# Optimization experiments

Hardware: AMD Instinct MI355X
Metric: run time of the kernel (lower is better)

## Reference

```python
import jax, jax.numpy as jnp
import numpy as np

B, T, D, H = 64, 512, 1024, 1024


def setup_inputs() -> dict:
    key = jax.random.key(0)
    k1, k2, k3 = jax.random.split(key, 3)
    scale = 0.02  # keep tanh out of saturation
    return {
        "x": jax.random.normal(k1, (B, T, D), dtype=jnp.float32),
        "Wi": jax.random.normal(k2, (H, D), dtype=jnp.float32) * scale,
        "bi": jnp.zeros((H,), dtype=jnp.float32),
        "Wh": jax.random.normal(k3, (H, H), dtype=jnp.float32) * scale,
        "bh": jnp.zeros((H,), dtype=jnp.float32),
    }


def reference(x, Wi, bi, Wh, bh):
    # x: [B, T, D]; torch Linear weights are [out, in].
    # Precompute the input projection as one big GEMM (faithful: Wi(x_t)+bi).
    xi = jnp.einsum("btd,hd->bth", x, Wi) + bi  # [B, T, H]

    def step(h, xt):
        # h: [B, H], xt: [B, H]
        h_new = jnp.tanh(xt + h @ Wh.T + bh)
        return h_new, h_new

    h0 = jnp.zeros((x.shape[0], Wh.shape[0]), dtype=x.dtype)
    _, hs = jax.lax.scan(step, h0, jnp.swapaxes(xi, 0, 1))  # [T, B, H]
    return jnp.swapaxes(hs, 0, 1)  # [B, T, H]
```

## Files before the change

kernel.cpp:

```cpp
#include <hip/hip_runtime.h>
#include <hip/hip_bf16.h>

#define B_ 64
#define T_ 512
#define D_ 1024
#define H_ 1024

typedef __bf16 bf16x8 __attribute__((ext_vector_type(8)));
typedef float f32x4 __attribute__((ext_vector_type(4)));

static __device__ __forceinline__ unsigned short f2bf(float f) {
  union { float f; unsigned u; } v; v.f = f;
  unsigned u = v.u;
  unsigned r = (u + 0x7fffu + ((u >> 16) & 1u)) >> 16;
  return (unsigned short)r;
}

__global__ __launch_bounds__(256) void xi_gemm(const float* __restrict__ x,
                                               const float* __restrict__ Wi,
                                               const float* __restrict__ bi,
                                               float* __restrict__ out) {
  __shared__ __align__(16) unsigned short As[128][40];
  __shared__ __align__(16) unsigned short Ws[128][40];
  const int tid = threadIdx.x;
  const int wave = tid >> 6;
  const int lane = tid & 63;
  const int wm = wave >> 1, wn = wave & 1;
  const int lr = lane & 15, lk = lane >> 4;
  const long row0 = (long)blockIdx.x * 128;
  const int col0 = (int)blockIdx.y * 128;

  f32x4 acc[4][4];
#pragma unroll
  for (int m = 0; m < 4; ++m)
#pragma unroll
    for (int n = 0; n < 4; ++n)
      acc[m][n] = (f32x4){0.f, 0.f, 0.f, 0.f};

  for (int kt = 0; kt < 32; ++kt) {
    __syncthreads();
#pragma unroll
    for (int it = 0; it < 4; ++it) {
      int i = tid + it * 256;
      int row = i >> 3, c = i & 7;
      float4 va = *reinterpret_cast<const float4*>(
          &x[(row0 + row) * 1024 + kt * 32 + c * 4]);
      ushort4 ba = {f2bf(va.x), f2bf(va.y), f2bf(va.z), f2bf(va.w)};
      *reinterpret_cast<ushort4*>(&As[row][c * 4]) = ba;
      float4 vw = *reinterpret_cast<const float4*>(
          &Wi[(long)(col0 + row) * 1024 + kt * 32 + c * 4]);
      ushort4 bw = {f2bf(vw.x), f2bf(vw.y), f2bf(vw.z), f2bf(vw.w)};
      *reinterpret_cast<ushort4*>(&Ws[row][c * 4]) = bw;
    }
    __syncthreads();
    bf16x8 af[4], wf[4];
#pragma unroll
    for (int m = 0; m < 4; ++m)
      af[m] = *reinterpret_cast<const bf16x8*>(&As[wm * 64 + m * 16 + lr][lk * 8]);
#pragma unroll
    for (int n = 0; n < 4; ++n)
      wf[n] = *reinterpret_cast<const bf16x8*>(&Ws[wn * 64 + n * 16 + lr][lk * 8]);
#pragma unroll
    for (int m = 0; m < 4; ++m)
#pragma unroll
      for (int n = 0; n < 4; ++n)
        acc[m][n] = __builtin_amdgcn_mfma_f32_16x16x32_bf16(af[m], wf[n], acc[m][n], 0, 0, 0);
  }
#pragma unroll
  for (int m = 0; m < 4; ++m) {
#pragma unroll
    for (int n = 0; n < 4; ++n) {
#pragma unroll
      for (int r = 0; r < 4; ++r) {
        long row = row0 + wm * 64 + m * 16 + lk * 4 + r;
        int col = col0 + wn * 64 + n * 16 + lr;
        out[row * 1024 + col] = acc[m][n][r] + bi[col];
      }
    }
  }
}

__global__ __launch_bounds__(64) void rnn_xcd(const float* __restrict__ Wh,
                                              const float* __restrict__ bh,
                                              float* __restrict__ out,
                                              unsigned* __restrict__ ctrs,
                                              unsigned* __restrict__ flagsF,
                                              unsigned* __restrict__ flagsB,
                                              unsigned short* __restrict__ hsF,
                                              unsigned short* __restrict__ hsB) {
  extern __shared__ __align__(16) unsigned short Whs[];
  const int lane = threadIdx.x;
  const int lr = lane & 15, lk = lane >> 4;

  unsigned xcc = 0, slot = 0, okv = 0;
  if (lane == 0) {
    xcc = __builtin_amdgcn_s_getreg((31u << 11) | 20u) & 15u;
    slot = __hip_atomic_fetch_add(&ctrs[xcc], 1u, __ATOMIC_RELAXED,
                                  __HIP_MEMORY_SCOPE_AGENT);
    __hip_atomic_fetch_add(&ctrs[16], 1u, __ATOMIC_RELEASE,
                           __HIP_MEMORY_SCOPE_AGENT);
    unsigned spin = 0;
    while (__hip_atomic_load(&ctrs[16], __ATOMIC_ACQUIRE,
                             __HIP_MEMORY_SCOPE_AGENT) < 256u) {
      __builtin_amdgcn_s_sleep(1);
      if (++spin > 2000000u) break;
    }
    unsigned ok = 1;
    for (int i = 0; i < 8; ++i)
      if (__hip_atomic_load(&ctrs[i], __ATOMIC_RELAXED,
                            __HIP_MEMORY_SCOPE_AGENT) != 32u) ok = 0;
    for (int i = 8; i < 16; ++i)
      if (__hip_atomic_load(&ctrs[i], __ATOMIC_RELAXED,
                            __HIP_MEMORY_SCOPE_AGENT) != 0u) ok = 0;
    okv = ok;
  }
  xcc  = (unsigned)__shfl((int)xcc, 0, 64);
  slot = (unsigned)__shfl((int)slot, 0, 64);
  okv  = (unsigned)__shfl((int)okv, 0, 64);

  if (okv) {
    const int j0 = (int)slot * 32;
#pragma unroll 8
    for (int it = 0; it < 128; ++it) {
      int i = lane + it * 64;
      int row = i >> 8, c = i & 255;
      float4 v = *reinterpret_cast<const float4*>(&Wh[(long)(j0 + row) * 1024 + c * 4]);
      ushort4 b4 = {f2bf(v.x), f2bf(v.y), f2bf(v.z), f2bf(v.w)};
      *reinterpret_cast<ushort4*>(&Whs[row * 1032 + c * 4]) = b4;
    }
    __syncthreads();

    const int jc0 = j0 + lr;
    const int jc1 = j0 + 16 + lr;
    const float bhv0 = bh[jc0], bhv1 = bh[jc1];
    const unsigned short* wb0 = &Whs[lr * 1032 + lk * 8];
    const unsigned short* wb1 = &Whs[(16 + lr) * 1032 + lk * 8];
    unsigned* hw = reinterpret_cast<unsigned*>(hsF);
    const unsigned fslot = (xcc * 32u + slot) << 4;

    for (int t = 0; t < T_; ++t) {
      float xr0[4], xr1[4];
      if (t > 0) {
        asm volatile("s_waitcnt vmcnt(0)" ::: "memory");
        if (lane == 0)
          __hip_atomic_store(&flagsF[fslot], (unsigned)t,
                             __ATOMIC_RELAXED, __HIP_MEMORY_SCOPE_AGENT);
        if (lk < 2) {
#pragma unroll
          for (int r = 0; r < 4; ++r) {
            size_t oi = ((size_t)(xcc * 8 + lk * 4 + r) * T_ + t) * H_;
            xr0[r] = out[oi + jc0];
            xr1[r] = out[oi + jc1];
          }
        }
        unsigned spin = 0;
        for (;;) {
          unsigned v = (unsigned)t;
          if (lane < 32)
            v = __hip_atomic_load(&flagsF[(xcc * 32u + (unsigned)lane) << 4],
                                  __ATOMIC_RELAXED, __HIP_MEMORY_SCOPE_AGENT);
          if (__all((int)(v >= (unsigned)t))) break;
          if (spin >= 2) __builtin_amdgcn_s_sleep(1);
          if (++spin > 50000u) break;
        }
        __builtin_amdgcn_fence(__ATOMIC_ACQUIRE, "agent");
      } else {
        if (lk < 2) {
#pragma unroll
          for (int r = 0; r < 4; ++r) {
            size_t oi = ((size_t)(xcc * 8 + lk * 4 + r) * T_ + t) * H_;
            xr0[r] = out[oi + jc0];
            xr1[r] = out[oi + jc1];
          }
        }
      }

      f32x4 a00 = {0,0,0,0}, a01 = {0,0,0,0}, a10 = {0,0,0,0}, a11 = {0,0,0,0};
      if (t > 0) {
        const unsigned short* hp = hsF + (size_t)xcc * 32768 +
                                   (size_t)((t - 1) & 1) * 16384 +
                                   (size_t)lr * 1024 + lk * 8;
#pragma unroll 4
        for (int ks = 0; ks < 16; ++ks) {
          bf16x8 ah0 = *reinterpret_cast<const bf16x8*>(hp + ks * 32);
          bf16x8 ah1 = *reinterpret_cast<const bf16x8*>(hp + (ks + 16) * 32);
          bf16x8 w00 = *reinterpret_cast<const bf16x8*>(wb0 + ks * 32);
          bf16x8 w01 = *reinterpret_cast<const bf16x8*>(wb0 + (ks + 16) * 32);
          bf16x8 w10 = *reinterpret_cast<const bf16x8*>(wb1 + ks * 32);
          bf16x8 w11 = *reinterpret_cast<const bf16x8*>(wb1 + (ks + 16) * 32);
          a00 = __builtin_amdgcn_mfma_f32_16x16x32_bf16(ah0, w00, a00, 0, 0, 0);
          a01 = __builtin_amdgcn_mfma_f32_16x16x32_bf16(ah1, w01, a01, 0, 0, 0);
          a10 = __builtin_amdgcn_mfma_f32_16x16x32_bf16(ah0, w10, a10, 0, 0, 0);
          a11 = __builtin_amdgcn_mfma_f32_16x16x32_bf16(ah1, w11, a11, 0, 0, 0);
        }
      }
      f32x4 acc0 = a00 + a01, acc1 = a10 + a11;

      const unsigned pw = (unsigned)(t & 1) * 8192u;
      if (lk < 2) {
#pragma unroll
        for (int r = 0; r < 4; ++r) {
          int row = lk * 4 + r;
          size_t oi = ((size_t)(xcc * 8 + row) * T_ + t) * H_;
          float h0 = tanhf(xr0[r] + acc0[r] + bhv0);
          float h1 = tanhf(xr1[r] + acc1[r] + bhv1);
          out[oi + jc0] = h0;
          out[oi + jc1] = h1;
          unsigned u0 = f2bf(h0), u1 = f2bf(h1);
          unsigned o0 = (unsigned)__shfl_xor((int)u0, 1, 64);
          unsigned o1 = (unsigned)__shfl_xor((int)u1, 1, 64);
          if ((lr & 1) == 0) {
            unsigned base = xcc * 16384u + pw + (unsigned)row * 512u;
            hw[base + ((unsigned)jc0 >> 1)] = u0 | (o0 << 16);
            hw[base + ((unsigned)jc1 >> 1)] = u1 | (o1 << 16);
          }
        }
      }
    }
  } else {
    const int bid = (int)blockIdx.x;
    const int jg = bid & 63, bg = bid >> 6;
    const int j0 = jg * 16, brow = bg * 16;
#pragma unroll 8
    for (int it = 0; it < 64; ++it) {
      int i = lane + it * 64;
      int row = i >> 8, c = i & 255;
      float4 v = *reinterpret_cast<const float4*>(&Wh[(long)(j0 + row) * 1024 + c * 4]);
      ushort4 b4 = {f2bf(v.x), f2bf(v.y), f2bf(v.z), f2bf(v.w)};
      *reinterpret_cast<ushort4*>(&Whs[row * 1032 + c * 4]) = b4;
    }
    __syncthreads();
    const int jcol = j0 + lr;
    const float bhv = bh[jcol];
    const unsigned short* wbl = &Whs[lr * 1032 + lk * 8];
    unsigned* hw = reinterpret_cast<unsigned*>(hsB);
    const int jp = jcol >> 1;

    for (int t = 0; t < T_; ++t) {
      if (t > 0) {
        asm volatile("s_waitcnt vmcnt(0)" ::: "memory");
        if (lane == 0)
          __hip_atomic_store(&flagsB[(unsigned)bid << 4], (unsigned)t,
                             __ATOMIC_RELAXED, __HIP_MEMORY_SCOPE_AGENT);
        unsigned spin = 0;
        for (;;) {
          unsigned va = __hip_atomic_load(&flagsB[(unsigned)lane << 4],
                                 __ATOMIC_RELAXED, __HIP_MEMORY_SCOPE_AGENT);
          unsigned vb = __hip_atomic_load(&flagsB[((unsigned)lane + 64u) << 4],
                                 __ATOMIC_RELAXED, __HIP_MEMORY_SCOPE_AGENT);
          unsigned vc = __hip_atomic_load(&flagsB[((unsigned)lane + 128u) << 4],
                                 __ATOMIC_RELAXED, __HIP_MEMORY_SCOPE_AGENT);
          unsigned vd = __hip_atomic_load(&flagsB[((unsigned)lane + 192u) << 4],
                                 __ATOMIC_RELAXED, __HIP_MEMORY_SCOPE_AGENT);
          int ok = (va >= (unsigned)t) && (vb >= (unsigned)t) &&
                   (vc >= (unsigned)t) && (vd >= (unsigned)t);
          if (__all(ok)) break;
          __builtin_amdgcn_s_sleep(2);
          if (++spin > 50000u) break;
        }
        __builtin_amdgcn_fence(__ATOMIC_ACQUIRE, "agent");
      }

      f32x4 a0 = {0,0,0,0}, a1 = {0,0,0,0};
      if (t > 0) {
        const unsigned short* hbl = hsB + (size_t)((t - 1) & 1) * 65536 +
                                    (size_t)(brow + lr) * 1024 + lk * 8;
#pragma unroll 4
        for (int ks = 0; ks < 16; ++ks) {
          bf16x8 ah0 = *reinterpret_cast<const bf16x8*>(hbl + ks * 32);
          bf16x8 ah1 = *reinterpret_cast<const bf16x8*>(hbl + (ks + 16) * 32);
          bf16x8 wf0 = *reinterpret_cast<const bf16x8*>(wbl + ks * 32);
          bf16x8 wf1 = *reinterpret_cast<const bf16x8*>(wbl + (ks + 16) * 32);
          a0 = __builtin_amdgcn_mfma_f32_16x16x32_bf16(ah0, wf0, a0, 0, 0, 0);
          a1 = __builtin_amdgcn_mfma_f32_16x16x32_bf16(ah1, wf1, a1, 0, 0, 0);
        }
      }
      f32x4 acc = a0 + a1;

      const unsigned pw = (unsigned)(t & 1) * 32768u;
#pragma unroll
      for (int r = 0; r < 4; ++r) {
        int b = brow + lk * 4 + r;
        size_t oi = ((size_t)b * T_ + t) * H_ + jcol;
        float z = out[oi] + acc[r] + bhv;
        float h = tanhf(z);
        out[oi] = h;
        unsigned hi_u = f2bf(h);
        unsigned o_hi = (unsigned)__shfl_xor((int)hi_u, 1, 64);
        if ((lr & 1) == 0) {
          __hip_atomic_store(&hw[pw + (unsigned)b * 512u + (unsigned)jp],
                             hi_u | (o_hi << 16),
                             __ATOMIC_RELAXED, __HIP_MEMORY_SCOPE_AGENT);
        }
      }
    }
  }
}

__global__ __launch_bounds__(256) void rnn_step(const float* __restrict__ Wh,
                                                const float* __restrict__ bh,
                                                float* __restrict__ out,
                                                int t) {
  const int bg = blockIdx.x & 3;
  const int jg = blockIdx.x >> 2;
  const int b = bg * 16 + (threadIdx.x >> 4);
  const int j = jg * 16 + (threadIdx.x & 15);
  float a0 = 0.f, a1 = 0.f, a2 = 0.f, a3 = 0.f;
  if (t > 0) {
    const float4* __restrict__ wr = reinterpret_cast<const float4*>(&Wh[(long)j * H_]);
    const float4* __restrict__ hr = reinterpret_cast<const float4*>(
        &out[((long)b * T_ + (t - 1)) * H_]);
#pragma unroll 8
    for (int kc = 0; kc < 256; ++kc) {
      float4 w = wr[kc];
      float4 h = hr[kc];
      a0 = fmaf(w.x, h.x, a0);
      a1 = fmaf(w.y, h.y, a1);
      a2 = fmaf(w.z, h.z, a2);
      a3 = fmaf(w.w, h.w, a3);
    }
  }
  const long oi = ((long)b * T_ + t) * H_ + j;
  float z = out[oi] + ((a0 + a1) + (a2 + a3)) + bh[j];
  out[oi] = tanhf(z);
}

extern "C" void kernel_launch(void* const* d_in, const int* in_sizes, int n_in,
                              void* d_out, int out_size, void* d_ws, size_t ws_size,
                              hipStream_t stream) {
  const float* x  = (const float*)d_in[0];
  const float* Wi = (const float*)d_in[1];
  const float* bi = (const float*)d_in[2];
  const float* Wh = (const float*)d_in[3];
  const float* bh = (const float*)d_in[4];
  float* out = (float*)d_out;

  const size_t CTRS_OFF  = 0;
  const size_t FLAGF_OFF = 4096;
  const size_t FLAGB_OFF = 20480;
  const size_t HSF_OFF   = 36864;
  const size_t HSB_OFF   = 561152;
  const size_t NEED      = HSB_OFF + 262144;

  hipLaunchKernelGGL(xi_gemm, dim3(256, 8), dim3(256), 0, stream, x, Wi, bi, out);

  bool launched = false;
  if (ws_size >= NEED) {
    unsigned* ctrs = (unsigned*)((char*)d_ws + CTRS_OFF);
    unsigned* flagsF = (unsigned*)((char*)d_ws + FLAGF_OFF);
    unsigned* flagsB = (unsigned*)((char*)d_ws + FLAGB_OFF);
    unsigned short* hsF = (unsigned short*)((char*)d_ws + HSF_OFF);
    unsigned short* hsB = (unsigned short*)((char*)d_ws + HSB_OFF);
    hipMemsetAsync(d_ws, 0, HSF_OFF + 524288, stream);

    const float* Wh_ = Wh; const float* bh_ = bh; float* out_ = out;
    void* args[] = {(void*)&Wh_, (void*)&bh_, (void*)&out_,
                    (void*)&ctrs, (void*)&flagsF, (void*)&flagsB,
                    (void*)&hsF, (void*)&hsB};
    const int lds = 32 * 1032 * 2;
    hipError_t e = hipFuncSetAttribute(
        reinterpret_cast<const void*>(rnn_xcd),
        hipFuncAttributeMaxDynamicSharedMemorySize, lds);
    if (e == hipSuccess)
      e = hipLaunchCooperativeKernel((void*)rnn_xcd, dim3(256), dim3(64),
                                     args, lds, stream);
    launched = (e == hipSuccess);
  }
  if (!launched) {
    for (int t = 0; t < T_; ++t)
      hipLaunchKernelGGL(rnn_step, dim3(256), dim3(256), 0, stream, Wh, bh, out, t);
  }
}
```

Before: 3.411 ms.

## Use two-wave blocks to halve per-XCD barrier participants in the recurrent kernel

The persistent recurrent kernel now runs 128 blocks of 128 threads instead of 256 single-wave blocks. Each block owns 64 hidden columns split across its two waves, so each XCD's per-step flag barrier has 16 participants instead of 32. The fallback path is remapped the same way and polls half as many flags. Within a block the waves now meet at __syncthreads before one thread publishes the step flag. The LDS row pitch also changes from 1032 to 1028 elements, which makes 16-byte fragment reads 8-byte aligned only, and the intra-block barrier adds a local sync each step.

```diff
diff --git a/kernel.cpp b/kernel.cpp
--- a/kernel.cpp
+++ b/kernel.cpp
@@ -80,69 +80,70 @@
   }
 }
 
-__global__ __launch_bounds__(64) void rnn_xcd(const float* __restrict__ Wh,
-                                              const float* __restrict__ bh,
-                                              float* __restrict__ out,
-                                              unsigned* __restrict__ ctrs,
-                                              unsigned* __restrict__ flagsF,
-                                              unsigned* __restrict__ flagsB,
-                                              unsigned short* __restrict__ hsF,
-                                              unsigned short* __restrict__ hsB) {
+__global__ __launch_bounds__(128) void rnn_xcd(const float* __restrict__ Wh,
+                                               const float* __restrict__ bh,
+                                               float* __restrict__ out,
+                                               unsigned* __restrict__ ctrs,
+                                               unsigned* __restrict__ flagsF,
+                                               unsigned* __restrict__ flagsB,
+                                               unsigned short* __restrict__ hsF,
+                                               unsigned short* __restrict__ hsB) {
   extern __shared__ __align__(16) unsigned short Whs[];
-  const int lane = threadIdx.x;
+  __shared__ unsigned meta[4];
+  const int tid = threadIdx.x;
+  const int wave = tid >> 6, lane = tid & 63;
   const int lr = lane & 15, lk = lane >> 4;
 
-  unsigned xcc = 0, slot = 0, okv = 0;
-  if (lane == 0) {
-    xcc = __builtin_amdgcn_s_getreg((31u << 11) | 20u) & 15u;
-    slot = __hip_atomic_fetch_add(&ctrs[xcc], 1u, __ATOMIC_RELAXED,
-                                  __HIP_MEMORY_SCOPE_AGENT);
+  if (tid == 0) {
+    unsigned xcc = __builtin_amdgcn_s_getreg((31u << 11) | 20u) & 15u;
+    unsigned slot = __hip_atomic_fetch_add(&ctrs[xcc], 1u, __ATOMIC_RELAXED,
+                                           __HIP_MEMORY_SCOPE_AGENT);
     __hip_atomic_fetch_add(&ctrs[16], 1u, __ATOMIC_RELEASE,
                            __HIP_MEMORY_SCOPE_AGENT);
     unsigned spin = 0;
     while (__hip_atomic_load(&ctrs[16], __ATOMIC_ACQUIRE,
-                             __HIP_MEMORY_SCOPE_AGENT) < 256u) {
+                             __HIP_MEMORY_SCOPE_AGENT) < 128u) {
       __builtin_amdgcn_s_sleep(1);
       if (++spin > 2000000u) break;
     }
     unsigned ok = 1;
     for (int i = 0; i < 8; ++i)
       if (__hip_atomic_load(&ctrs[i], __ATOMIC_RELAXED,
-                            __HIP_MEMORY_SCOPE_AGENT) != 32u) ok = 0;
+                            __HIP_MEMORY_SCOPE_AGENT) != 16u) ok = 0;
     for (int i = 8; i < 16; ++i)
       if (__hip_atomic_load(&ctrs[i], __ATOMIC_RELAXED,
                             __HIP_MEMORY_SCOPE_AGENT) != 0u) ok = 0;
-    okv = ok;
-  }
-  xcc  = (unsigned)__shfl((int)xcc, 0, 64);
-  slot = (unsigned)__shfl((int)slot, 0, 64);
-  okv  = (unsigned)__shfl((int)okv, 0, 64);
+    meta[0] = xcc; meta[1] = slot; meta[2] = ok;
+  }
+  __syncthreads();
+  const unsigned xcc = meta[0], slot = meta[1], okv = meta[2];
 
   if (okv) {
-    const int j0 = (int)slot * 32;
+    const int j0 = (int)slot * 64;
 #pragma unroll 8
     for (int it = 0; it < 128; ++it) {
-      int i = lane + it * 64;
+      int i = tid + it * 128;
       int row = i >> 8, c = i & 255;
       float4 v = *reinterpret_cast<const float4*>(&Wh[(long)(j0 + row) * 1024 + c * 4]);
       ushort4 b4 = {f2bf(v.x), f2bf(v.y), f2bf(v.z), f2bf(v.w)};
-      *reinterpret_cast<ushort4*>(&Whs[row * 1032 + c * 4]) = b4;
+      *reinterpret_cast<ushort4*>(&Whs[row * 1028 + c * 4]) = b4;
     }
     __syncthreads();
 
-    const int jc0 = j0 + lr;
-    const int jc1 = j0 + 16 + lr;
+    const int wcol = wave * 32;
+    const int jc0 = j0 + wcol + lr;
+    const int jc1 = jc0 + 16;
     const float bhv0 = bh[jc0], bhv1 = bh[jc1];
-    const unsigned short* wb0 = &Whs[lr * 1032 + lk * 8];
-    const unsigned short* wb1 = &Whs[(16 + lr) * 1032 + lk * 8];
+    const unsigned short* wb0 = &Whs[(wcol + lr) * 1028 + lk * 8];
+    const unsigned short* wb1 = &Whs[(wcol + 16 + lr) * 1028 + lk * 8];
     unsigned* hw = reinterpret_cast<unsigned*>(hsF);
-    const unsigned fslot = (xcc * 32u + slot) << 4;
+    const unsigned fslot = (xcc * 16u + slot) << 4;
 
     for (int t = 0; t < T_; ++t) {
       float xr0[4], xr1[4];
       if (t > 0) {
-        asm volatile("s_waitcnt vmcnt(0)" ::: "memory");
-        if (lane == 0)
+        __syncthreads();
+        if (tid == 0)
           __hip_atomic_store(&flagsF[fslot], (unsigned)t,
                              __ATOMIC_RELAXED, __HIP_MEMORY_SCOPE_AGENT);
         if (lk < 2) {
@@ -156,11 +157,11 @@
         unsigned spin = 0;
         for (;;) {
           unsigned v = (unsigned)t;
-          if (lane < 32)
-            v = __hip_atomic_load(&flagsF[(xcc * 32u + (unsigned)lane) << 4],
+          if (lane < 16)
+            v = __hip_atomic_load(&flagsF[(xcc * 16u + (unsigned)lane) << 4],
                                   __ATOMIC_RELAXED, __HIP_MEMORY_SCOPE_AGENT);
           if (__all((int)(v >= (unsigned)t))) break;
-          if (spin >= 2) __builtin_amdgcn_s_sleep(1);
+          if (spin >= 8) __builtin_amdgcn_s_sleep(1);
           if (++spin > 50000u) break;
         }
         __builtin_amdgcn_fence(__ATOMIC_ACQUIRE, "agent");
@@ -218,29 +219,29 @@
       }
     }
   } else {
-    const int bid = (int)blockIdx.x;
-    const int jg = bid & 63, bg = bid >> 6;
-    const int j0 = jg * 16, brow = bg * 16;
+    const int vbid = (int)blockIdx.x * 2 + wave;
+    const int jg = vbid & 63, bg = vbid >> 6;
+    const int j0f = jg * 16, brow = bg * 16;
 #pragma unroll 8
     for (int it = 0; it < 64; ++it) {
       int i = lane + it * 64;
       int row = i >> 8, c = i & 255;
-      float4 v = *reinterpret_cast<const float4*>(&Wh[(long)(j0 + row) * 1024 + c * 4]);
+      float4 v = *reinterpret_cast<const float4*>(&Wh[(long)(j0f + row) * 1024 + c * 4]);
       ushort4 b4 = {f2bf(v.x), f2bf(v.y), f2bf(v.z), f2bf(v.w)};
-      *reinterpret_cast<ushort4*>(&Whs[row * 1032 + c * 4]) = b4;
+      *reinterpret_cast<ushort4*>(&Whs[(wave * 16 + row) * 1028 + c * 4]) = b4;
     }
     __syncthreads();
-    const int jcol = j0 + lr;
+    const int jcol = j0f + lr;
     const float bhv = bh[jcol];
-    const unsigned short* wbl = &Whs[lr * 1032 + lk * 8];
+    const unsigned short* wbl = &Whs[(wave * 16 + lr) * 1028 + lk * 8];
     unsigned* hw = reinterpret_cast<unsigned*>(hsB);
     const int jp = jcol >> 1;
 
     for (int t = 0; t < T_; ++t) {
       if (t > 0) {
-        asm volatile("s_waitcnt vmcnt(0)" ::: "memory");
-        if (lane == 0)
-          __hip_atomic_store(&flagsB[(unsigned)bid << 4], (unsigned)t,
+        __syncthreads();
+        if (tid == 0)
+          __hip_atomic_store(&flagsB[(unsigned)blockIdx.x << 4], (unsigned)t,
                              __ATOMIC_RELAXED, __HIP_MEMORY_SCOPE_AGENT);
         unsigned spin = 0;
         for (;;) {
@@ -248,12 +249,7 @@
                                  __ATOMIC_RELAXED, __HIP_MEMORY_SCOPE_AGENT);
           unsigned vb = __hip_atomic_load(&flagsB[((unsigned)lane + 64u) << 4],
                                  __ATOMIC_RELAXED, __HIP_MEMORY_SCOPE_AGENT);
-          unsigned vc = __hip_atomic_load(&flagsB[((unsigned)lane + 128u) << 4],
-                                 __ATOMIC_RELAXED, __HIP_MEMORY_SCOPE_AGENT);
-          unsigned vd = __hip_atomic_load(&flagsB[((unsigned)lane + 192u) << 4],
-                                 __ATOMIC_RELAXED, __HIP_MEMORY_SCOPE_AGENT);
-          int ok = (va >= (unsigned)t) && (vb >= (unsigned)t) &&
-                   (vc >= (unsigned)t) && (vd >= (unsigned)t);
+          int ok = (va >= (unsigned)t) && (vb >= (unsigned)t);
           if (__all(ok)) break;
           __builtin_amdgcn_s_sleep(2);
           if (++spin > 50000u) break;
@@ -357,12 +353,12 @@
     void* args[] = {(void*)&Wh_, (void*)&bh_, (void*)&out_,
                     (void*)&ctrs, (void*)&flagsF, (void*)&flagsB,
                     (void*)&hsF, (void*)&hsB};
-    const int lds = 32 * 1032 * 2;
+    const int lds = 64 * 1028 * 2;
     hipError_t e = hipFuncSetAttribute(
         reinterpret_cast<const void*>(rnn_xcd),
         hipFuncAttributeMaxDynamicSharedMemorySize, lds);
     if (e == hipSuccess)
-      e = hipLaunchCooperativeKernel((void*)rnn_xcd, dim3(256), dim3(64),
+      e = hipLaunchCooperativeKernel((void*)rnn_xcd, dim3(128), dim3(128),
                                      args, lds, stream);
     launched = (e == hipSuccess);
   }
```

Measured after the change: 3.910 ms. 1.15x slower.
